# Performance work log

Hardware: AMD Instinct MI355X
Metric: run time of the kernel (lower is better)

## Reference

```python
import jax, jax.numpy as jnp
import numpy as np

EPS = 1e-8  # torch.nn.CosineSimilarity default eps


def setup_inputs() -> dict:
    key = jax.random.key(0)
    k1, k2 = jax.random.split(key)
    B, D = 2048, 512
    return {
        "z_i": jax.random.normal(k1, (B, D), dtype=jnp.float32),
        "z_j": jax.random.normal(k2, (B, D), dtype=jnp.float32),
        "temperature": 0.5,
    }


def _neg_mask_indices(B):
    # static (numpy) mask: remove diagonal and the two +/-B positive diagonals
    N = 2 * B
    mask = np.ones((N, N), dtype=bool)
    np.fill_diagonal(mask, False)
    idx = np.arange(B)
    mask[idx, idx + B] = False
    mask[idx + B, idx] = False
    rows, cols = np.where(mask)  # each row keeps exactly N-2 entries, row-major order
    return rows, cols


def reference(z_i, z_j, temperature):
    B = z_i.shape[0]
    N = 2 * B
    z = jnp.concatenate([z_i, z_j], axis=0)                      # [N, D]
    # cosine similarity = normalized GEMM (same math as pairwise CosineSimilarity)
    zn = z / jnp.maximum(jnp.linalg.norm(z, axis=1, keepdims=True), EPS)
    sim = jnp.matmul(zn, zn.T) / temperature                      # [N, N]

    pos = jnp.concatenate([jnp.diagonal(sim, B), jnp.diagonal(sim, -B)])[:, None]  # [N, 1]
    rows, cols = _neg_mask_indices(B)
    neg = sim[rows, cols].reshape(N, N - 2)                       # [N, N-2]

    logits = jnp.concatenate([pos, neg], axis=1)                  # [N, N-1], label = 0
    # sum-reduced cross-entropy with label 0, divided by N
    loss = jnp.sum(jax.nn.logsumexp(logits, axis=1) - logits[:, 0]) / N

    # avg_rank: position of the positive (column 0) in descending sort of logits
    order = jnp.argsort(-logits, axis=1)
    avg_rank = jnp.mean(jnp.argmin(order, axis=1).astype(jnp.float32))
    return loss, avg_rank
```

## Files before the change

### kernel.cpp

```cpp
#include <hip/hip_runtime.h>
#include <math.h>

#define DDIM 512
#define BT 64
#define NT 64
#define NTILES (NT * (NT + 1) / 2)
#define NSL 16
#define NCH 64

typedef __attribute__((ext_vector_type(4))) float f32x4;

__device__ __forceinline__ unsigned char f2e4m3(float x) {
  unsigned ux = __builtin_bit_cast(unsigned, x);
  unsigned sign = (ux >> 24) & 0x80u;
  float a = fminf(fabsf(x), 448.f);
  unsigned ua = __builtin_bit_cast(unsigned, a);
  int E = (int)((ua >> 23) & 0xff);
  if (E == 0) return (unsigned char)sign;
  E -= 127;
  int t = E - 3; if (t < -9) t = -9;
  float c = __builtin_bit_cast(float, (unsigned)((t + 150) << 23));
  float r = (a + c) - c;
  if (r <= 0.f) return (unsigned char)sign;
  unsigned ur = __builtin_bit_cast(unsigned, r);
  int Er = (int)((ur >> 23) & 0xff) - 127;
  if (Er < -6) {
    unsigned man = (unsigned)(r * 512.f + 0.5f);
    return (unsigned char)(sign | man);
  }
  unsigned man = (ur >> 20) & 7u;
  return (unsigned char)(sign | ((unsigned)(Er + 7) << 3) | man);
}
__device__ __forceinline__ float e4m32f(unsigned char b) {
  int e = (b >> 3) & 0xf, m = b & 7;
  float v = (e == 0) ? (float)m * 0.001953125f
                     : (float)(8 + m) * __builtin_bit_cast(float, (unsigned)((e + 117) << 23));
  return (b & 0x80) ? -v : v;
}

__device__ __forceinline__ size_t frag_off(int rt, int s, int lane) {
  return ((size_t)(rt * NSL + s) * 64 + lane) * 8;
}

__global__ void k_prep(const float* __restrict__ zi, const float* __restrict__ zj,
                       const float* __restrict__ tempp,
                       unsigned char* __restrict__ zf, float* __restrict__ pos,
                       int B) {
  int wv = (blockIdx.x * blockDim.x + threadIdx.x) >> 6;
  int lane = threadIdx.x & 63;
  if (wv >= B) return;
  const float* a = zi + (size_t)wv * DDIM;
  const float* b = zj + (size_t)wv * DDIM;
  float4 a0 = *(const float4*)(a + lane * 8);
  float4 a1 = *(const float4*)(a + lane * 8 + 4);
  float4 b0 = *(const float4*)(b + lane * 8);
  float4 b1 = *(const float4*)(b + lane * 8 + 4);
  float av[8] = {a0.x, a0.y, a0.z, a0.w, a1.x, a1.y, a1.z, a1.w};
  float bv[8] = {b0.x, b0.y, b0.z, b0.w, b1.x, b1.y, b1.z, b1.w};
  float sa = 0.f, sb = 0.f;
#pragma unroll
  for (int i = 0; i < 8; ++i) { sa = fmaf(av[i], av[i], sa); sb = fmaf(bv[i], bv[i], sb); }
#pragma unroll
  for (int off = 32; off; off >>= 1) { sa += __shfl_xor(sa, off, 64); sb += __shfl_xor(sb, off, 64); }
  float ia = 1.f / fmaxf(sqrtf(sa), 1e-8f);
  float ib = 1.f / fmaxf(sqrtf(sb), 1e-8f);
  unsigned long long pa = 0ull, pb = 0ull;
  float fa[8], fb[8];
#pragma unroll
  for (int i = 0; i < 8; ++i) {
    unsigned char qa = f2e4m3(av[i] * ia); fa[i] = e4m32f(qa);
    unsigned char qb = f2e4m3(bv[i] * ib); fb[i] = e4m32f(qb);
    pa |= ((unsigned long long)qa) << (8 * i);
    pb |= ((unsigned long long)qb) << (8 * i);
  }
  const int s = lane >> 2, g = lane & 3;
  {
    int r = wv;
    *(unsigned long long*)(zf + frag_off(r >> 4, s, (g << 4) | (r & 15))) = pa;
    r = wv + B;
    *(unsigned long long*)(zf + frag_off(r >> 4, s, (g << 4) | (r & 15))) = pb;
  }
  float pd = 0.f;
#pragma unroll
  for (int i = 0; i < 8; ++i) pd = fmaf(fa[i], fb[i], pd);
#pragma unroll
  for (int off = 32; off; off >>= 1) pd += __shfl_xor(pd, off, 64);
  if (lane == 0) {
    float p = pd / tempp[0];
    pos[wv] = p; pos[wv + B] = p;
  }
}

__global__ __launch_bounds__(64) void k_main(
    const unsigned char* __restrict__ zf, const float* __restrict__ pos,
    const float* __restrict__ tempp, float* __restrict__ partS,
    float* __restrict__ partC, int B) {
  int tri = (blockIdx.x & 7) * (NTILES / 8) + (blockIdx.x >> 3);
  int bi = 0;
  while (tri >= NT - bi) { tri -= NT - bi; ++bi; }
  const int bj = bi + tri;
  const int r0 = bi * BT, c0 = bj * BT;
  const bool diag = (bi == bj);
  const float invt = 1.0f / tempp[0];

  const int lane = threadIdx.x;
  const int cl = lane & 15, g = lane >> 4;
  const int art = r0 >> 4;
  const int brt = c0 >> 4;

  f32x4 acc[4][4];
#pragma unroll
  for (int m = 0; m < 4; ++m)
#pragma unroll
    for (int n = 0; n < 4; ++n) acc[m][n] = (f32x4){0.f, 0.f, 0.f, 0.f};

#pragma unroll 4
  for (int s = 0; s < NSL; ++s) {
    long long aF[4], bF[4];
#pragma unroll
    for (int m = 0; m < 4; ++m)
      aF[m] = *(const long long*)(zf + frag_off(art + m, s, lane));
#pragma unroll
    for (int n = 0; n < 4; ++n)
      bF[n] = *(const long long*)(zf + frag_off(brt + n, s, lane));
#pragma unroll
    for (int m = 0; m < 4; ++m)
#pragma unroll
      for (int n = 0; n < 4; ++n)
        acc[m][n] = __builtin_amdgcn_mfma_f32_16x16x32_fp8_fp8(aF[m], bF[n], acc[m][n], 0, 0, 0);
  }

  int growv[16], gpartr[16];
  float pvr[16];
#pragma unroll
  for (int m = 0; m < 4; ++m)
#pragma unroll
    for (int reg = 0; reg < 4; ++reg) {
      int idx = m * 4 + reg;
      int grow = r0 + m * 16 + g * 4 + reg;
      growv[idx] = grow;
      gpartr[idx] = (grow < B) ? grow + B : grow - B;
      pvr[idx] = pos[grow];
    }
  int gcolv[4], gpartc[4];
  float pvc[4];
#pragma unroll
  for (int n = 0; n < 4; ++n) {
    int gcol = c0 + n * 16 + cl;
    gcolv[n] = gcol;
    gpartc[n] = (gcol < B) ? gcol + B : gcol - B;
    pvc[n] = pos[gcol];
  }

  float ssr[16], ccr[16], ssc[4], ccc[4];
#pragma unroll
  for (int i = 0; i < 16; ++i) { ssr[i] = 0.f; ccr[i] = 0.f; }
#pragma unroll
  for (int n = 0; n < 4; ++n) { ssc[n] = 0.f; ccc[n] = 0.f; }

#pragma unroll
  for (int m = 0; m < 4; ++m)
#pragma unroll
    for (int n = 0; n < 4; ++n)
#pragma unroll
      for (int reg = 0; reg < 4; ++reg) {
        const int idx = m * 4 + reg;
        float val = acc[m][n][reg] * invt;
        float e = __expf(val);
        bool isd = diag && (gcolv[n] == growv[idx]);
        if (!isd) {
          ssr[idx] += e;
          ccr[idx] += (gcolv[n] != gpartr[idx] && val > pvr[idx]) ? 1.f : 0.f;
        }
        if (!diag) {
          ssc[n] += e;
          ccc[n] += (growv[idx] != gpartc[n] && val > pvc[n]) ? 1.f : 0.f;
        }
      }

#pragma unroll
  for (int idx = 0; idx < 16; ++idx) {
    float s = ssr[idx], c = ccr[idx];
#pragma unroll
    for (int off = 1; off < 16; off <<= 1) {
      s += __shfl_xor(s, off, 64);
      c += __shfl_xor(c, off, 64);
    }
    if (cl == 0) {
      partS[(size_t)growv[idx] * NCH + bj] = s;
      partC[(size_t)growv[idx] * NCH + bj] = c;
    }
  }
  if (!diag) {
#pragma unroll
    for (int n = 0; n < 4; ++n) {
      float s = ssc[n], c = ccc[n];
      s += __shfl_xor(s, 16, 64); c += __shfl_xor(c, 16, 64);
      s += __shfl_xor(s, 32, 64); c += __shfl_xor(c, 32, 64);
      if (g == 0) {
        partS[(size_t)gcolv[n] * NCH + bi] = s;
        partC[(size_t)gcolv[n] * NCH + bi] = c;
      }
    }
  }
}

__global__ void k_rowfin(const float* __restrict__ partS, const float* __restrict__ partC,
                         const float* __restrict__ pos, float* __restrict__ rowL,
                         float* __restrict__ rowC, int N) {
  int r = (blockIdx.x * blockDim.x + threadIdx.x) >> 6;
  int lane = threadIdx.x & 63;
  if (r >= N) return;
  float s = partS[(size_t)r * NCH + lane];
  float c = partC[(size_t)r * NCH + lane];
#pragma unroll
  for (int off = 32; off; off >>= 1) { s += __shfl_xor(s, off, 64); c += __shfl_xor(c, off, 64); }
  if (lane == 0) {
    rowL[r] = logf(s) - pos[r];
    rowC[r] = c;
  }
}

__global__ void k_final(const float* __restrict__ rowL, const float* __restrict__ rowC,
                        float* __restrict__ out, int N) {
  float ls = 0.f, cs = 0.f;
  for (int r = threadIdx.x; r < N; r += 256) { ls += rowL[r]; cs += rowC[r]; }
  __shared__ float l[256], c[256];
  l[threadIdx.x] = ls; c[threadIdx.x] = cs;
  __syncthreads();
  for (int off = 128; off; off >>= 1) {
    if (threadIdx.x < off) { l[threadIdx.x] += l[threadIdx.x + off]; c[threadIdx.x] += c[threadIdx.x + off]; }
    __syncthreads();
  }
  if (threadIdx.x == 0) { out[0] = l[0] / (float)N; out[1] = c[0] / (float)N; }
}

extern "C" void kernel_launch(void* const* d_in, const int* in_sizes, int n_in,
                              void* d_out, int out_size, void* d_ws, size_t ws_size,
                              hipStream_t stream) {
  const float* zi = (const float*)d_in[0];
  const float* zj = (const float*)d_in[1];
  const float* temp = (const float*)d_in[2];
  float* out = (float*)d_out;

  const int B = in_sizes[0] / DDIM;
  const int N = 2 * B;

  unsigned char* zf = (unsigned char*)d_ws;
  float* fws = (float*)(zf + (size_t)N * DDIM);
  float* pos   = fws;
  float* partS = pos + N;
  float* partC = partS + (size_t)N * NCH;
  float* rowL  = partC + (size_t)N * NCH;
  float* rowC  = rowL + N;

  k_prep<<<(B * 64) / 256, 256, 0, stream>>>(zi, zj, temp, zf, pos, B);
  k_main<<<NTILES, 64, 0, stream>>>(zf, pos, temp, partS, partC, B);
  k_rowfin<<<(N * 64) / 256, 256, 0, stream>>>(partS, partC, pos, rowL, rowC, N);
  k_final<<<1, 256, 0, stream>>>(rowL, rowC, out, N);
}
```

Baseline: 48.83 us.

## Split each 64x64 tile across four waves with shared-memory column reduction

```diff
diff --git a/kernel.cpp b/kernel.cpp
--- a/kernel.cpp
+++ b/kernel.cpp
@@ -91,7 +91,7 @@
   }
 }
 
-__global__ __launch_bounds__(64) void k_main(
+__global__ __launch_bounds__(256) void k_main(
     const unsigned char* __restrict__ zf, const float* __restrict__ pos,
     const float* __restrict__ tempp, float* __restrict__ partS,
     float* __restrict__ partC, int B) {
@@ -103,45 +103,38 @@
   const bool diag = (bi == bj);
   const float invt = 1.0f / tempp[0];
 
-  const int lane = threadIdx.x;
+  const int t = threadIdx.x;
+  const int lane = t & 63;
+  const int wave = t >> 6;
   const int cl = lane & 15, g = lane >> 4;
-  const int art = r0 >> 4;
+  const int art = (r0 >> 4) + wave;
   const int brt = c0 >> 4;
 
-  f32x4 acc[4][4];
-#pragma unroll
-  for (int m = 0; m < 4; ++m)
-#pragma unroll
-    for (int n = 0; n < 4; ++n) acc[m][n] = (f32x4){0.f, 0.f, 0.f, 0.f};
-
-#pragma unroll 4
+  f32x4 acc[4];
+#pragma unroll
+  for (int n = 0; n < 4; ++n) acc[n] = (f32x4){0.f, 0.f, 0.f, 0.f};
+
+#pragma unroll 2
   for (int s = 0; s < NSL; ++s) {
-    long long aF[4], bF[4];
-#pragma unroll
-    for (int m = 0; m < 4; ++m)
-      aF[m] = *(const long long*)(zf + frag_off(art + m, s, lane));
+    long long aF = *(const long long*)(zf + frag_off(art, s, lane));
+    long long bF[4];
 #pragma unroll
     for (int n = 0; n < 4; ++n)
       bF[n] = *(const long long*)(zf + frag_off(brt + n, s, lane));
 #pragma unroll
-    for (int m = 0; m < 4; ++m)
-#pragma unroll
-      for (int n = 0; n < 4; ++n)
-        acc[m][n] = __builtin_amdgcn_mfma_f32_16x16x32_fp8_fp8(aF[m], bF[n], acc[m][n], 0, 0, 0);
-  }
-
-  int growv[16], gpartr[16];
-  float pvr[16];
-#pragma unroll
-  for (int m = 0; m < 4; ++m)
-#pragma unroll
-    for (int reg = 0; reg < 4; ++reg) {
-      int idx = m * 4 + reg;
-      int grow = r0 + m * 16 + g * 4 + reg;
-      growv[idx] = grow;
-      gpartr[idx] = (grow < B) ? grow + B : grow - B;
-      pvr[idx] = pos[grow];
-    }
+    for (int n = 0; n < 4; ++n)
+      acc[n] = __builtin_amdgcn_mfma_f32_16x16x32_fp8_fp8(aF, bF[n], acc[n], 0, 0, 0);
+  }
+
+  int growv[4], gpartr[4];
+  float pvr[4];
+#pragma unroll
+  for (int reg = 0; reg < 4; ++reg) {
+    int grow = r0 + wave * 16 + g * 4 + reg;
+    growv[reg] = grow;
+    gpartr[reg] = (grow < B) ? grow + B : grow - B;
+    pvr[reg] = pos[grow];
+  }
   int gcolv[4], gpartc[4];
   float pvc[4];
 #pragma unroll
@@ -152,56 +145,62 @@
     pvc[n] = pos[gcol];
   }
 
-  float ssr[16], ccr[16], ssc[4], ccc[4];
-#pragma unroll
-  for (int i = 0; i < 16; ++i) { ssr[i] = 0.f; ccr[i] = 0.f; }
-#pragma unroll
-  for (int n = 0; n < 4; ++n) { ssc[n] = 0.f; ccc[n] = 0.f; }
-
-#pragma unroll
-  for (int m = 0; m < 4; ++m)
-#pragma unroll
-    for (int n = 0; n < 4; ++n)
-#pragma unroll
-      for (int reg = 0; reg < 4; ++reg) {
-        const int idx = m * 4 + reg;
-        float val = acc[m][n][reg] * invt;
-        float e = __expf(val);
-        bool isd = diag && (gcolv[n] == growv[idx]);
-        if (!isd) {
-          ssr[idx] += e;
-          ccr[idx] += (gcolv[n] != gpartr[idx] && val > pvr[idx]) ? 1.f : 0.f;
-        }
-        if (!diag) {
-          ssc[n] += e;
-          ccc[n] += (growv[idx] != gpartc[n] && val > pvc[n]) ? 1.f : 0.f;
-        }
+  float ssr[4], ccr[4], ssc[4], ccc[4];
+#pragma unroll
+  for (int i = 0; i < 4; ++i) { ssr[i] = 0.f; ccr[i] = 0.f; ssc[i] = 0.f; ccc[i] = 0.f; }
+
+#pragma unroll
+  for (int n = 0; n < 4; ++n)
+#pragma unroll
+    for (int reg = 0; reg < 4; ++reg) {
+      float val = acc[n][reg] * invt;
+      float e = __expf(val);
+      bool isd = diag && (gcolv[n] == growv[reg]);
+      if (!isd) {
+        ssr[reg] += e;
+        ccr[reg] += (gcolv[n] != gpartr[reg] && val > pvr[reg]) ? 1.f : 0.f;
       }
-
-#pragma unroll
-  for (int idx = 0; idx < 16; ++idx) {
-    float s = ssr[idx], c = ccr[idx];
+      if (!diag) {
+        ssc[n] += e;
+        ccc[n] += (growv[reg] != gpartc[n] && val > pvc[n]) ? 1.f : 0.f;
+      }
+    }
+
+#pragma unroll
+  for (int reg = 0; reg < 4; ++reg) {
+    float s = ssr[reg], c = ccr[reg];
 #pragma unroll
     for (int off = 1; off < 16; off <<= 1) {
       s += __shfl_xor(s, off, 64);
       c += __shfl_xor(c, off, 64);
     }
     if (cl == 0) {
-      partS[(size_t)growv[idx] * NCH + bj] = s;
-      partC[(size_t)growv[idx] * NCH + bj] = c;
-    }
-  }
+      partS[(size_t)growv[reg] * NCH + bj] = s;
+      partC[(size_t)growv[reg] * NCH + bj] = c;
+    }
+  }
+
+  __shared__ float colS[256], colC[256];
   if (!diag) {
 #pragma unroll
     for (int n = 0; n < 4; ++n) {
-      float s = ssc[n], c = ccc[n];
-      s += __shfl_xor(s, 16, 64); c += __shfl_xor(c, 16, 64);
-      s += __shfl_xor(s, 32, 64); c += __shfl_xor(c, 32, 64);
-      if (g == 0) {
-        partS[(size_t)gcolv[n] * NCH + bi] = s;
-        partC[(size_t)gcolv[n] * NCH + bi] = c;
+      ssc[n] += __shfl_xor(ssc[n], 16, 64); ccc[n] += __shfl_xor(ccc[n], 16, 64);
+      ssc[n] += __shfl_xor(ssc[n], 32, 64); ccc[n] += __shfl_xor(ccc[n], 32, 64);
+    }
+    if (g == 0) {
+#pragma unroll
+      for (int n = 0; n < 4; ++n) {
+        colS[wave * 64 + n * 16 + cl] = ssc[n];
+        colC[wave * 64 + n * 16 + cl] = ccc[n];
       }
     }
+  }
+  __syncthreads();
+  if (!diag && t < 64) {
+    float s = colS[t] + colS[64 + t] + colS[128 + t] + colS[192 + t];
+    float c = colC[t] + colC[64 + t] + colC[128 + t] + colC[192 + t];
+    partS[(size_t)(c0 + t) * NCH + bi] = s;
+    partC[(size_t)(c0 + t) * NCH + bi] = c;
   }
 }
 
@@ -255,7 +254,7 @@
   float* rowC  = rowL + N;
 
   k_prep<<<(B * 64) / 256, 256, 0, stream>>>(zi, zj, temp, zf, pos, B);
-  k_main<<<NTILES, 64, 0, stream>>>(zf, pos, temp, partS, partC, B);
+  k_main<<<NTILES, 256, 0, stream>>>(zf, pos, temp, partS, partC, B);
   k_rowfin<<<(N * 64) / 256, 256, 0, stream>>>(partS, partC, pos, rowL, rowC, N);
   k_final<<<1, 256, 0, stream>>>(rowL, rowC, out, N);
 }
```

New measurement: 48.25 us. Within noise of the previous version (-1.2%).

## Use 128x128 tiles with four waves, wider fp8 fragment loads, fused finalize

Applied to the files above, without the earlier changes.

```diff
diff --git a/kernel.cpp b/kernel.cpp
--- a/kernel.cpp
+++ b/kernel.cpp
@@ -2,10 +2,10 @@
 #include <math.h>
 
 #define DDIM 512
-#define BT 64
-#define NT 64
+#define BT 128
+#define NT 32
 #define NTILES (NT * (NT + 1) / 2)
-#define NSL 16
+#define NSLP 8
 #define NCH 64
 
 typedef __attribute__((ext_vector_type(4))) float f32x4;
@@ -38,14 +38,18 @@
   return (b & 0x80) ? -v : v;
 }
 
-__device__ __forceinline__ size_t frag_off(int rt, int s, int lane) {
-  return ((size_t)(rt * NSL + s) * 64 + lane) * 8;
+__device__ __forceinline__ size_t chunk_off(int rt, int u) {
+  return ((size_t)(rt * NSLP + u)) << 10;
 }
 
 __global__ void k_prep(const float* __restrict__ zi, const float* __restrict__ zj,
                        const float* __restrict__ tempp,
                        unsigned char* __restrict__ zf, float* __restrict__ pos,
-                       int B) {
+                       float* __restrict__ accum, int B) {
+  if (blockIdx.x == 0 && threadIdx.x == 0) {
+    accum[0] = 0.f; accum[1] = 0.f;
+    *(unsigned*)(accum + 2) = 0u;
+  }
   int wv = (blockIdx.x * blockDim.x + threadIdx.x) >> 6;
   int lane = threadIdx.x & 63;
   if (wv >= B) return;
@@ -73,12 +77,12 @@
     pa |= ((unsigned long long)qa) << (8 * i);
     pb |= ((unsigned long long)qb) << (8 * i);
   }
-  const int s = lane >> 2, g = lane & 3;
+  const int u = lane >> 3, h = (lane >> 2) & 1, g = lane & 3;
   {
     int r = wv;
-    *(unsigned long long*)(zf + frag_off(r >> 4, s, (g << 4) | (r & 15))) = pa;
+    *(unsigned long long*)(zf + chunk_off(r >> 4, u) + (((g << 4) | (r & 15)) * 16 + h * 8)) = pa;
     r = wv + B;
-    *(unsigned long long*)(zf + frag_off(r >> 4, s, (g << 4) | (r & 15))) = pb;
+    *(unsigned long long*)(zf + chunk_off(r >> 4, u) + (((g << 4) | (r & 15)) * 16 + h * 8)) = pb;
   }
   float pd = 0.f;
 #pragma unroll
@@ -91,7 +95,7 @@
   }
 }
 
-__global__ __launch_bounds__(64) void k_main(
+__global__ __launch_bounds__(256) void k_main(
     const unsigned char* __restrict__ zf, const float* __restrict__ pos,
     const float* __restrict__ tempp, float* __restrict__ partS,
     float* __restrict__ partC, int B) {
@@ -103,10 +107,14 @@
   const bool diag = (bi == bj);
   const float invt = 1.0f / tempp[0];
 
-  const int lane = threadIdx.x;
+  const int t = threadIdx.x;
+  const int lane = t & 63;
+  const int wave = t >> 6;
+  const int wr = wave >> 1, wc = wave & 1;
   const int cl = lane & 15, g = lane >> 4;
-  const int art = r0 >> 4;
-  const int brt = c0 >> 4;
+
+  const int art0 = (r0 >> 4) + wr * 4;
+  const int brt0 = (c0 >> 4) + wc * 4;
 
   f32x4 acc[4][4];
 #pragma unroll
@@ -114,20 +122,27 @@
 #pragma unroll
     for (int n = 0; n < 4; ++n) acc[m][n] = (f32x4){0.f, 0.f, 0.f, 0.f};
 
-#pragma unroll 4
-  for (int s = 0; s < NSL; ++s) {
-    long long aF[4], bF[4];
+#pragma unroll 2
+  for (int u = 0; u < NSLP; ++u) {
+    ulonglong2 aV[4], bV[4];
 #pragma unroll
     for (int m = 0; m < 4; ++m)
-      aF[m] = *(const long long*)(zf + frag_off(art + m, s, lane));
+      aV[m] = *(const ulonglong2*)(zf + chunk_off(art0 + m, u) + lane * 16);
 #pragma unroll
     for (int n = 0; n < 4; ++n)
-      bF[n] = *(const long long*)(zf + frag_off(brt + n, s, lane));
+      bV[n] = *(const ulonglong2*)(zf + chunk_off(brt0 + n, u) + lane * 16);
 #pragma unroll
     for (int m = 0; m < 4; ++m)
 #pragma unroll
       for (int n = 0; n < 4; ++n)
-        acc[m][n] = __builtin_amdgcn_mfma_f32_16x16x32_fp8_fp8(aF[m], bF[n], acc[m][n], 0, 0, 0);
+        acc[m][n] = __builtin_amdgcn_mfma_f32_16x16x32_fp8_fp8(
+            (long long)aV[m].x, (long long)bV[n].x, acc[m][n], 0, 0, 0);
+#pragma unroll
+    for (int m = 0; m < 4; ++m)
+#pragma unroll
+      for (int n = 0; n < 4; ++n)
+        acc[m][n] = __builtin_amdgcn_mfma_f32_16x16x32_fp8_fp8(
+            (long long)aV[m].y, (long long)bV[n].y, acc[m][n], 0, 0, 0);
   }
 
   int growv[16], gpartr[16];
@@ -137,7 +152,7 @@
 #pragma unroll
     for (int reg = 0; reg < 4; ++reg) {
       int idx = m * 4 + reg;
-      int grow = r0 + m * 16 + g * 4 + reg;
+      int grow = r0 + wr * 64 + m * 16 + g * 4 + reg;
       growv[idx] = grow;
       gpartr[idx] = (grow < B) ? grow + B : grow - B;
       pvr[idx] = pos[grow];
@@ -146,7 +161,7 @@
   float pvc[4];
 #pragma unroll
   for (int n = 0; n < 4; ++n) {
-    int gcol = c0 + n * 16 + cl;
+    int gcol = c0 + wc * 64 + n * 16 + cl;
     gcolv[n] = gcol;
     gpartc[n] = (gcol < B) ? gcol + B : gcol - B;
     pvc[n] = pos[gcol];
@@ -178,6 +193,7 @@
         }
       }
 
+  const int chR = bj * 2 + wc;
 #pragma unroll
   for (int idx = 0; idx < 16; ++idx) {
     float s = ssr[idx], c = ccr[idx];
@@ -187,52 +203,60 @@
       c += __shfl_xor(c, off, 64);
     }
     if (cl == 0) {
-      partS[(size_t)growv[idx] * NCH + bj] = s;
-      partC[(size_t)growv[idx] * NCH + bj] = c;
+      partS[(size_t)growv[idx] * NCH + chR] = s;
+      partC[(size_t)growv[idx] * NCH + chR] = c;
     }
   }
   if (!diag) {
+    const int chC = bi * 2 + wr;
 #pragma unroll
     for (int n = 0; n < 4; ++n) {
       float s = ssc[n], c = ccc[n];
       s += __shfl_xor(s, 16, 64); c += __shfl_xor(c, 16, 64);
       s += __shfl_xor(s, 32, 64); c += __shfl_xor(c, 32, 64);
       if (g == 0) {
-        partS[(size_t)gcolv[n] * NCH + bi] = s;
-        partC[(size_t)gcolv[n] * NCH + bi] = c;
+        partS[(size_t)gcolv[n] * NCH + chC] = s;
+        partC[(size_t)gcolv[n] * NCH + chC] = c;
       }
     }
   }
 }
 
-__global__ void k_rowfin(const float* __restrict__ partS, const float* __restrict__ partC,
-                         const float* __restrict__ pos, float* __restrict__ rowL,
-                         float* __restrict__ rowC, int N) {
-  int r = (blockIdx.x * blockDim.x + threadIdx.x) >> 6;
-  int lane = threadIdx.x & 63;
-  if (r >= N) return;
-  float s = partS[(size_t)r * NCH + lane];
-  float c = partC[(size_t)r * NCH + lane];
-#pragma unroll
-  for (int off = 32; off; off >>= 1) { s += __shfl_xor(s, off, 64); c += __shfl_xor(c, off, 64); }
-  if (lane == 0) {
-    rowL[r] = logf(s) - pos[r];
-    rowC[r] = c;
-  }
-}
-
-__global__ void k_final(const float* __restrict__ rowL, const float* __restrict__ rowC,
-                        float* __restrict__ out, int N) {
-  float ls = 0.f, cs = 0.f;
-  for (int r = threadIdx.x; r < N; r += 256) { ls += rowL[r]; cs += rowC[r]; }
-  __shared__ float l[256], c[256];
-  l[threadIdx.x] = ls; c[threadIdx.x] = cs;
+__global__ __launch_bounds__(256) void k_fin(
+    const float* __restrict__ partS, const float* __restrict__ partC,
+    const float* __restrict__ pos, float* __restrict__ accum,
+    float* __restrict__ out, int N) {
+  const int lane = threadIdx.x & 63;
+  const int wave = threadIdx.x >> 6;
+  float lsum = 0.f, csum = 0.f;
+#pragma unroll 4
+  for (int i = 0; i < 16; ++i) {
+    int r = blockIdx.x * 64 + wave * 16 + i;
+    float s = partS[(size_t)r * NCH + lane];
+    float c = partC[(size_t)r * NCH + lane];
+#pragma unroll
+    for (int off = 32; off; off >>= 1) {
+      s += __shfl_xor(s, off, 64);
+      c += __shfl_xor(c, off, 64);
+    }
+    lsum += logf(s) - pos[r];
+    csum += c;
+  }
+  __shared__ float ls[4], cs[4];
+  if (lane == 0) { ls[wave] = lsum; cs[wave] = csum; }
   __syncthreads();
-  for (int off = 128; off; off >>= 1) {
-    if (threadIdx.x < off) { l[threadIdx.x] += l[threadIdx.x + off]; c[threadIdx.x] += c[threadIdx.x + off]; }
-    __syncthreads();
-  }
-  if (threadIdx.x == 0) { out[0] = l[0] / (float)N; out[1] = c[0] / (float)N; }
+  if (threadIdx.x == 0) {
+    atomicAdd(&accum[0], ls[0] + ls[1] + ls[2] + ls[3]);
+    atomicAdd(&accum[1], cs[0] + cs[1] + cs[2] + cs[3]);
+    __threadfence();
+    unsigned old = atomicAdd((unsigned*)(accum + 2), 1u);
+    if (old == (unsigned)(gridDim.x - 1)) {
+      float lt = atomicAdd(&accum[0], 0.f);
+      float ct = atomicAdd(&accum[1], 0.f);
+      out[0] = lt / (float)N;
+      out[1] = ct / (float)N;
+    }
+  }
 }
 
 extern "C" void kernel_launch(void* const* d_in, const int* in_sizes, int n_in,
@@ -251,11 +275,9 @@
   float* pos   = fws;
   float* partS = pos + N;
   float* partC = partS + (size_t)N * NCH;
-  float* rowL  = partC + (size_t)N * NCH;
-  float* rowC  = rowL + N;
-
-  k_prep<<<(B * 64) / 256, 256, 0, stream>>>(zi, zj, temp, zf, pos, B);
-  k_main<<<NTILES, 64, 0, stream>>>(zf, pos, temp, partS, partC, B);
-  k_rowfin<<<(N * 64) / 256, 256, 0, stream>>>(partS, partC, pos, rowL, rowC, N);
-  k_final<<<1, 256, 0, stream>>>(rowL, rowC, out, N);
-}
+  float* accum = partC + (size_t)N * NCH;
+
+  k_prep<<<(B * 64) / 256, 256, 0, stream>>>(zi, zj, temp, zf, pos, accum, B);
+  k_main<<<NTILES, 256, 0, stream>>>(zf, pos, temp, partS, partC, B);
+  k_fin<<<64, 256, 0, stream>>>(partS, partC, pos, accum, out, N);
+}
```

After: 54.90 us. +12.4%, slower.
